# Kernel tuning notes

Hardware: AMD Instinct MI355X
Metric: run time of the kernel (lower is better)

## Reference

```python
import jax, jax.numpy as jnp
import numpy as np

EMB = 512
HEAD = 8
HEAD_DIM = EMB // HEAD


def setup_inputs() -> dict:
    key = jax.random.key(0)
    ks = jax.random.split(key, 12)
    B, S = 2, 4096
    scale = 1.0 / np.sqrt(EMB)
    inp = {
        "q": jax.random.normal(ks[0], (B, S, EMB), dtype=jnp.float32),
        "kv": jax.random.normal(ks[1], (B, S, EMB), dtype=jnp.float32),
        "Wq": jax.random.normal(ks[2], (EMB, EMB), dtype=jnp.float32) * scale,
        "bq": jax.random.normal(ks[3], (EMB,), dtype=jnp.float32) * 0.01,
        "Wk": jax.random.normal(ks[4], (EMB, EMB), dtype=jnp.float32) * scale,
        "bk": jax.random.normal(ks[5], (EMB,), dtype=jnp.float32) * 0.01,
        "Wv": jax.random.normal(ks[6], (EMB, EMB), dtype=jnp.float32) * scale,
        "bv": jax.random.normal(ks[7], (EMB,), dtype=jnp.float32) * 0.01,
        "Wo": jax.random.normal(ks[8], (EMB, EMB), dtype=jnp.float32) * scale,
        "bo": jax.random.normal(ks[9], (EMB,), dtype=jnp.float32) * 0.01,
    }
    return inp


def reference(q, kv, Wq, bq, Wk, bk, Wv, bv, Wo, bo):
    B, N, _ = q.shape
    M = kv.shape[1]
    # Linear projections (torch Linear: x @ W^T + b)
    qh = (q @ Wq.T + bq).reshape(B, N, HEAD, HEAD_DIM).transpose(0, 2, 1, 3)  # [B,H,N,d]
    kh = (kv @ Wk.T + bk).reshape(B, M, HEAD, HEAD_DIM).transpose(0, 2, 1, 3)  # [B,H,M,d]
    vh = (kv @ Wv.T + bv).reshape(B, M, HEAD, HEAD_DIM).transpose(0, 2, 1, 3)  # [B,H,M,d]
    attn = jnp.einsum("bhnd,bhmd->bhnm", qh, kh) / jnp.sqrt(jnp.float32(HEAD_DIM))
    attn = jax.nn.softmax(attn, axis=-1)
    out = jnp.einsum("bhnm,bhmd->bhnd", attn, vh)  # [B,H,N,d]
    out = out.transpose(0, 2, 1, 3).reshape(B, N, EMB)
    out = out @ Wo.T + bo
    return out
```

## Files before the change

kernel.cpp:

```cpp
#include <hip/hip_runtime.h>
#include <stdint.h>

typedef unsigned short u16;
typedef __attribute__((ext_vector_type(8))) short short8;
typedef __attribute__((ext_vector_type(4))) float f32x4;
typedef __attribute__((ext_vector_type(16))) float f32x16;

typedef __attribute__((address_space(1))) void as1_void;
typedef __attribute__((address_space(3))) void as3_void;

__device__ inline u16 f2bf(float x) {
  uint32_t u = __float_as_uint(x);
  return (u16)((u + 0x7fffu + ((u >> 16) & 1u)) >> 16);
}

__device__ inline void gload16(const void* g, void* l) {
  __builtin_amdgcn_global_load_lds((as1_void*)g, (as3_void*)l, 16, 0, 0);
}

__device__ inline uint32_t cvtpk(float lo, float hi) {
  uint32_t d;
  asm("v_cvt_pk_bf16_f32 %0, %1, %2" : "=v"(d) : "v"(lo), "v"(hi));
  return d;
}

__device__ inline void plswap(uint32_t& a, uint32_t& b) {
  asm("v_permlane32_swap_b32 %0, %1" : "+v"(a), "+v"(b));
}

__device__ inline float fexp2(float x) {
  float r;
  asm("v_exp_f32 %0, %1" : "=v"(r) : "v"(x));
  return r;
}

__global__ __launch_bounds__(256) void cvt_all(const float* __restrict__ q,
                                               const float* __restrict__ kv,
                                               const float* __restrict__ Wq,
                                               const float* __restrict__ Wk,
                                               const float* __restrict__ Wv,
                                               const float* __restrict__ Wo,
                                               u16* __restrict__ qb,
                                               u16* __restrict__ kvb,
                                               u16* __restrict__ wall) {
  const int bx = blockIdx.x;
  const float* in;
  u16* out;
  int i;
  if (bx < 4096) {
    in = q; out = qb; i = bx * 256 + threadIdx.x;
  } else if (bx < 8192) {
    in = kv; out = kvb; i = (bx - 4096) * 256 + threadIdx.x;
  } else {
    int widx = (bx - 8192) >> 8;
    in = (widx == 0) ? Wq : (widx == 1) ? Wk : (widx == 2) ? Wv : Wo;
    out = wall + (size_t)widx * 262144;
    i = ((bx - 8192) & 255) * 256 + threadIdx.x;
  }
  float4 v = ((const float4*)in)[i];
  ushort4 o;
  o.x = f2bf(v.x); o.y = f2bf(v.y); o.z = f2bf(v.z); o.w = f2bf(v.w);
  ((ushort4*)out)[i] = o;
}

__global__ __launch_bounds__(256) void gemm_qkv(const u16* __restrict__ qb,
                                                const u16* __restrict__ kvb,
                                                const u16* __restrict__ wq,
                                                const u16* __restrict__ wk,
                                                const u16* __restrict__ wv,
                                                const float* __restrict__ bq,
                                                const float* __restrict__ bk,
                                                const float* __restrict__ bv,
                                                u16* __restrict__ Qh,
                                                u16* __restrict__ Kh,
                                                u16* __restrict__ Vt, float qscale) {
  __shared__ u16 Al[128 * 32];
  __shared__ u16 Wl[128 * 32];
  const int z = blockIdx.z;
  const u16* A = (z == 0) ? qb : kvb;
  const u16* W = (z == 0) ? wq : (z == 1) ? wk : wv;
  const float* bias = (z == 0) ? bq : (z == 1) ? bk : bv;
  const float prescale = (z == 0) ? qscale : 1.0f;
  u16* Cout = (z == 0) ? Qh : (z == 1) ? Kh : Vt;

  const int tid = threadIdx.x;
  const int lane = tid & 63;
  const int wv_ = tid >> 6;
  const int c = lane & 15;
  const int g = lane >> 4;
  const int wr = wv_ >> 1, wc = wv_ & 1;
  const int m0 = blockIdx.x * 128;
  const int n0 = blockIdx.y * 128;

  f32x4 acc[4][4];
#pragma unroll
  for (int i = 0; i < 4; i++)
#pragma unroll
    for (int j = 0; j < 4; j++) acc[i][j] = (f32x4){0.f, 0.f, 0.f, 0.f};

  for (int kk = 0; kk < 512; kk += 32) {
    __syncthreads();
    {
      int t0 = tid;
      int r0 = t0 >> 2, c0 = t0 & 3;
      gload16(A + (size_t)(m0 + r0) * 512 + kk + c0 * 8, (char*)Al + (size_t)(wv_ * 64) * 16);
      gload16(W + (size_t)(n0 + r0) * 512 + kk + c0 * 8, (char*)Wl + (size_t)(wv_ * 64) * 16);
      int t1 = 256 + tid;
      int r1 = t1 >> 2, c1 = t1 & 3;
      gload16(A + (size_t)(m0 + r1) * 512 + kk + c1 * 8, (char*)Al + (size_t)(256 + wv_ * 64) * 16);
      gload16(W + (size_t)(n0 + r1) * 512 + kk + c1 * 8, (char*)Wl + (size_t)(256 + wv_ * 64) * 16);
    }
    __syncthreads();

    short8 af[4], wf[4];
#pragma unroll
    for (int ai = 0; ai < 4; ai++)
      af[ai] = *(const short8*)&Al[(wr * 64 + ai * 16 + c) * 32 + g * 8];
#pragma unroll
    for (int bj = 0; bj < 4; bj++)
      wf[bj] = *(const short8*)&Wl[(wc * 64 + bj * 16 + c) * 32 + g * 8];
#pragma unroll
    for (int ai = 0; ai < 4; ai++)
#pragma unroll
      for (int bj = 0; bj < 4; bj++)
        acc[ai][bj] = __builtin_amdgcn_mfma_f32_16x16x32_bf16(af[ai], wf[bj], acc[ai][bj], 0, 0, 0);
  }

#pragma unroll
  for (int ai = 0; ai < 4; ai++)
#pragma unroll
    for (int bj = 0; bj < 4; bj++)
#pragma unroll
      for (int r = 0; r < 4; r++) {
        int m = m0 + wr * 64 + ai * 16 + g * 4 + r;
        int n = n0 + wc * 64 + bj * 16 + c;
        float v = (acc[ai][bj][r] + bias[n]) * prescale;
        int b = m >> 12, s = m & 4095;
        int h = n >> 6, d = n & 63;
        size_t idx;
        if (z < 2)
          idx = ((size_t)(b * 8 + h) * 4096 + s) * 64 + d;
        else
          idx = ((size_t)(b * 8 + h) * 64 + d) * 4096 + s;
        Cout[idx] = f2bf(v);
      }
}

__global__ __launch_bounds__(256) void gemm_out(const u16* __restrict__ A,
                                                const u16* __restrict__ W,
                                                const float* __restrict__ bias,
                                                float* __restrict__ Cout) {
  __shared__ u16 Al[128 * 32];
  __shared__ u16 Wl[128 * 32];
  const int tid = threadIdx.x;
  const int lane = tid & 63;
  const int wv_ = tid >> 6;
  const int c = lane & 15;
  const int g = lane >> 4;
  const int wr = wv_ >> 1, wc = wv_ & 1;
  const int m0 = blockIdx.x * 128;
  const int n0 = blockIdx.y * 128;

  f32x4 acc[4][4];
#pragma unroll
  for (int i = 0; i < 4; i++)
#pragma unroll
    for (int j = 0; j < 4; j++) acc[i][j] = (f32x4){0.f, 0.f, 0.f, 0.f};

  for (int kk = 0; kk < 512; kk += 32) {
    __syncthreads();
    {
      int t0 = tid;
      int r0 = t0 >> 2, c0 = t0 & 3;
      gload16(A + (size_t)(m0 + r0) * 512 + kk + c0 * 8, (char*)Al + (size_t)(wv_ * 64) * 16);
      gload16(W + (size_t)(n0 + r0) * 512 + kk + c0 * 8, (char*)Wl + (size_t)(wv_ * 64) * 16);
      int t1 = 256 + tid;
      int r1 = t1 >> 2, c1 = t1 & 3;
      gload16(A + (size_t)(m0 + r1) * 512 + kk + c1 * 8, (char*)Al + (size_t)(256 + wv_ * 64) * 16);
      gload16(W + (size_t)(n0 + r1) * 512 + kk + c1 * 8, (char*)Wl + (size_t)(256 + wv_ * 64) * 16);
    }
    __syncthreads();

    short8 af[4], wf[4];
#pragma unroll
    for (int ai = 0; ai < 4; ai++)
      af[ai] = *(const short8*)&Al[(wr * 64 + ai * 16 + c) * 32 + g * 8];
#pragma unroll
    for (int bj = 0; bj < 4; bj++)
      wf[bj] = *(const short8*)&Wl[(wc * 64 + bj * 16 + c) * 32 + g * 8];
#pragma unroll
    for (int ai = 0; ai < 4; ai++)
#pragma unroll
      for (int bj = 0; bj < 4; bj++)
        acc[ai][bj] = __builtin_amdgcn_mfma_f32_16x16x32_bf16(af[ai], wf[bj], acc[ai][bj], 0, 0, 0);
  }

#pragma unroll
  for (int ai = 0; ai < 4; ai++)
#pragma unroll
    for (int bj = 0; bj < 4; bj++)
#pragma unroll
      for (int r = 0; r < 4; r++) {
        int m = m0 + wr * 64 + ai * 16 + g * 4 + r;
        int n = n0 + wc * 64 + bj * 16 + c;
        Cout[(size_t)m * 512 + n] = acc[ai][bj][r] + bias[n];
      }
}

__global__ __launch_bounds__(256) void attn_split(const u16* __restrict__ Qh,
                                                  const u16* __restrict__ Kh,
                                                  const u16* __restrict__ Vt,
                                                  float* __restrict__ Op,
                                                  float* __restrict__ Ml) {
  __shared__ __align__(16) char smem[32768];
  const int tid = threadIdx.x;
  const int lane = tid & 63;
  const int w = tid >> 6;
  const int c5 = lane & 31;
  const int h = lane >> 5;
  const int bid = (blockIdx.x & 7) * 128 + (blockIdx.x >> 3);
  const int half = bid & 1;
  const int qt = (bid >> 1) & 31;
  const int bh = bid >> 6;
  const int q0 = qt * 128 + w * 32;
  const u16* Qb = Qh + (size_t)bh * 262144;
  const u16* Kb = Kh + (size_t)bh * 262144 + (size_t)half * 2048 * 64;
  const u16* Vb = Vt + (size_t)bh * 262144 + half * 2048;

  short8 qf[4];
#pragma unroll
  for (int kd = 0; kd < 4; kd++)
    qf[kd] = *(const short8*)(Qb + (size_t)(q0 + c5) * 64 + kd * 16 + h * 8);

  f32x16 accO[2];
#pragma unroll
  for (int i = 0; i < 16; i++) { accO[0][i] = 0.f; accO[1][i] = 0.f; }
  float l_r = 0.f;

  const int r = tid >> 4, p = tid & 15;
  const int x = p ^ r;
  const int gb = x >> 3, ge = x & 7;
  const u16* srcKA = Kb + (size_t)(r + 32 * gb) * 64 + ge * 8;
  const u16* srcKB = Kb + (size_t)(16 + r + 32 * gb) * 64 + ge * 8;
  const u16* srcVA = Vb + (size_t)(r + 32 * gb) * 4096 + ge * 8;
  const u16* srcVB = Vb + (size_t)(16 + r + 32 * gb) * 4096 + ge * 8;

#define ATTN_STAGE(BUF, T)                                \
  {                                                       \
    char* b_ = (char*)smem + (BUF)*16384 + w * 1024;      \
    gload16(srcKA + (size_t)(T)*4096, b_);                \
    gload16(srcKB + (size_t)(T)*4096, b_ + 4096);         \
    gload16(srcVA + (T)*64, b_ + 8192);                   \
    gload16(srcVB + (T)*64, b_ + 12288);                  \
  }

  ATTN_STAGE(0, 0)
  __syncthreads();
  const int swz = c5 & 15;
  const int rowb = c5 * 128;

  short8 pa_prev[4];
  short8 vf_prev[8];

  for (int t = 0; t < 32; ++t) {
    const int cur = t & 1;
    if (t < 31) ATTN_STAGE(cur ^ 1, t + 1)

    const u16* Kl = (const u16*)(smem + cur * 16384);
    const u16* Vl = Kl + 4096;

    f32x16 s0, s1;
#pragma unroll
    for (int i = 0; i < 16; i++) { s0[i] = 0.f; s1[i] = 0.f; }
    __builtin_amdgcn_s_setprio(1);
#pragma unroll
    for (int kd = 0; kd < 4; kd++) {
      short8 kf0 = *(const short8*)&Kl[rowb + ((((kd << 1) + h) ^ swz) << 3)];
      short8 kf1 = *(const short8*)&Kl[rowb + (((8 + (kd << 1) + h) ^ swz) << 3)];
      s0 = __builtin_amdgcn_mfma_f32_32x32x16_bf16(kf0, qf[kd], s0, 0, 0, 0);
      s1 = __builtin_amdgcn_mfma_f32_32x32x16_bf16(kf1, qf[kd], s1, 0, 0, 0);
    }
    if (t > 0) {
#pragma unroll
      for (int km = 0; km < 4; km++) {
        accO[0] = __builtin_amdgcn_mfma_f32_32x32x16_bf16(vf_prev[2 * km], pa_prev[km], accO[0], 0, 0, 0);
        accO[1] = __builtin_amdgcn_mfma_f32_32x32x16_bf16(vf_prev[2 * km + 1], pa_prev[km], accO[1], 0, 0, 0);
      }
    }
    __builtin_amdgcn_s_setprio(0);
    __builtin_amdgcn_sched_barrier(0);

#pragma unroll
    for (int i = 0; i < 16; i++) { s0[i] = fexp2(s0[i]); s1[i] = fexp2(s1[i]); }

    float tsum0 = ((s0[0] + s1[0]) + (s0[4] + s1[4])) + ((s0[8] + s1[8]) + (s0[12] + s1[12]));
    float tsum1 = ((s0[1] + s1[1]) + (s0[5] + s1[5])) + ((s0[9] + s1[9]) + (s0[13] + s1[13]));
    float tsum2 = ((s0[2] + s1[2]) + (s0[6] + s1[6])) + ((s0[10] + s1[10]) + (s0[14] + s1[14]));
    float tsum3 = ((s0[3] + s1[3]) + (s0[7] + s1[7])) + ((s0[11] + s1[11]) + (s0[15] + s1[15]));
    float rsq = (tsum0 + tsum1) + (tsum2 + tsum3);
    l_r += rsq + __shfl_xor(rsq, 32);

    uint32_t pk0[4][2], pk1[4][2];
#pragma unroll
    for (int u = 0; u < 4; u++) {
      pk0[u][0] = cvtpk(s0[4 * u], s0[4 * u + 1]);
      pk0[u][1] = cvtpk(s0[4 * u + 2], s0[4 * u + 3]);
      pk1[u][0] = cvtpk(s1[4 * u], s1[4 * u + 1]);
      pk1[u][1] = cvtpk(s1[4 * u + 2], s1[4 * u + 3]);
    }
#pragma unroll
    for (int km = 0; km < 2; km++) {
      const int uA = (km & 1) * 2, uB = uA + 1;
      uint32_t a0 = pk0[uA][0], b0 = pk0[uB][0]; plswap(a0, b0);
      uint32_t a1 = pk0[uA][1], b1 = pk0[uB][1]; plswap(a1, b1);
      union { uint32_t u[4]; short8 s; } uu;
      uu.u[0] = a0; uu.u[1] = a1; uu.u[2] = b0; uu.u[3] = b1;
      pa_prev[km] = uu.s;
    }
#pragma unroll
    for (int km = 2; km < 4; km++) {
      const int uA = (km & 1) * 2, uB = uA + 1;
      uint32_t a0 = pk1[uA][0], b0 = pk1[uB][0]; plswap(a0, b0);
      uint32_t a1 = pk1[uA][1], b1 = pk1[uB][1]; plswap(a1, b1);
      union { uint32_t u[4]; short8 s; } uu;
      uu.u[0] = a0; uu.u[1] = a1; uu.u[2] = b0; uu.u[3] = b1;
      pa_prev[km] = uu.s;
    }

#pragma unroll
    for (int km = 0; km < 4; km++) {
      vf_prev[2 * km]     = *(const short8*)&Vl[rowb + ((((km << 1) + h) ^ swz) << 3)];
      vf_prev[2 * km + 1] = *(const short8*)&Vl[rowb + (((8 + (km << 1) + h) ^ swz) << 3)];
    }

    __syncthreads();
  }

#pragma unroll
  for (int km = 0; km < 4; km++) {
    accO[0] = __builtin_amdgcn_mfma_f32_32x32x16_bf16(vf_prev[2 * km], pa_prev[km], accO[0], 0, 0, 0);
    accO[1] = __builtin_amdgcn_mfma_f32_32x32x16_bf16(vf_prev[2 * km + 1], pa_prev[km], accO[1], 0, 0, 0);
  }

  const size_t pbase = (size_t)(half * 16 + bh) * 4096 + q0 + c5;
  float* Opw = Op + pbase * 64;
#pragma unroll
  for (int db = 0; db < 2; db++)
#pragma unroll
    for (int rr = 0; rr < 16; rr++) {
      int d = db * 32 + 4 * h + (rr & 3) + 8 * (rr >> 2);
      Opw[d] = accO[db][rr];
    }
  if (h == 0) { Ml[pbase * 2] = 0.f; Ml[pbase * 2 + 1] = l_r; }
}

__global__ __launch_bounds__(256) void attn_combine(const float* __restrict__ Op,
                                                    const float* __restrict__ Ml,
                                                    u16* __restrict__ aO) {
  int tg = blockIdx.x * 256 + threadIdx.x;
  int bhq = tg >> 3, seg = tg & 7;
  const float* p0 = Op + (size_t)bhq * 64 + seg * 8;
  const float* p1 = p0 + 4194304;
  float m0 = Ml[bhq * 2], l0 = Ml[bhq * 2 + 1];
  float m1 = Ml[131072 + bhq * 2], l1 = Ml[131072 + bhq * 2 + 1];
  float ms = fmaxf(m0, m1);
  float a0 = fexp2(m0 - ms), a1 = fexp2(m1 - ms);
  float inv = 1.f / (l0 * a0 + l1 * a1);
  float4 x0 = ((const float4*)p0)[0], x1 = ((const float4*)p0)[1];
  float4 y0 = ((const float4*)p1)[0], y1 = ((const float4*)p1)[1];
  ushort4 o0, o1;
  o0.x = f2bf((x0.x * a0 + y0.x * a1) * inv);
  o0.y = f2bf((x0.y * a0 + y0.y * a1) * inv);
  o0.z = f2bf((x0.z * a0 + y0.z * a1) * inv);
  o0.w = f2bf((x0.w * a0 + y0.w * a1) * inv);
  o1.x = f2bf((x1.x * a0 + y1.x * a1) * inv);
  o1.y = f2bf((x1.y * a0 + y1.y * a1) * inv);
  o1.z = f2bf((x1.z * a0 + y1.z * a1) * inv);
  o1.w = f2bf((x1.w * a0 + y1.w * a1) * inv);
  int bh = bhq >> 12, q = bhq & 4095;
  int b = bh >> 3, hh = bh & 7;
  u16* dst = aO + ((size_t)(b * 4096 + q)) * 512 + hh * 64 + seg * 8;
  ((ushort4*)dst)[0] = o0;
  ((ushort4*)dst)[1] = o1;
}

extern "C" void kernel_launch(void* const* d_in, const int* in_sizes, int n_in,
                              void* d_out, int out_size, void* d_ws, size_t ws_size,
                              hipStream_t stream) {
  const float* q  = (const float*)d_in[0];
  const float* kv = (const float*)d_in[1];
  const float* Wq = (const float*)d_in[2];
  const float* bq = (const float*)d_in[3];
  const float* Wk = (const float*)d_in[4];
  const float* bk = (const float*)d_in[5];
  const float* Wv = (const float*)d_in[6];
  const float* bv = (const float*)d_in[7];
  const float* Wo = (const float*)d_in[8];
  const float* bo = (const float*)d_in[9];

  const size_t MB = 1u << 20;
  char* ws = (char*)d_ws;
  u16* qb  = (u16*)(ws + 0 * MB);
  u16* kvb = (u16*)(ws + 8 * MB);
  u16* wqb = (u16*)(ws + 16 * MB);
  u16* wkb = (u16*)(ws + 16 * MB + 524288);
  u16* wvb = (u16*)(ws + 17 * MB);
  u16* wob = (u16*)(ws + 17 * MB + 524288);
  u16* Qh  = (u16*)(ws + 18 * MB);
  u16* Kh  = (u16*)(ws + 26 * MB);
  u16* Vt  = (u16*)(ws + 34 * MB);
  u16* aO  = (u16*)(ws + 42 * MB);
  float* Op = (float*)(ws + 50 * MB);
  float* Ml = (float*)(ws + 84 * MB);

  cvt_all<<<dim3(9216), dim3(256), 0, stream>>>(q, kv, Wq, Wk, Wv, Wo, qb, kvb, wqb);

  const float qscale = 0.125f * 1.44269504088896340736f;
  gemm_qkv<<<dim3(64, 4, 3), dim3(256), 0, stream>>>(qb, kvb, wqb, wkb, wvb,
                                                     bq, bk, bv, Qh, Kh, Vt, qscale);

  attn_split<<<dim3(1024), dim3(256), 0, stream>>>(Qh, Kh, Vt, Op, Ml);
  attn_combine<<<dim3(2048), dim3(256), 0, stream>>>(Op, Ml, aO);

  gemm_out<<<dim3(64, 4), dim3(256), 0, stream>>>(aO, wob, bo, (float*)d_out);
}
```

Measured before the change: 142.6 us.

## Double-buffer GEMM K loop with swizzled LDS and smaller M tiles

Both projection GEMMs now prefetch the next 64-wide K slice into a second LDS buffer while computing on the current one, so each iteration needs one barrier instead of two. The shared tiles use an XOR swizzle to avoid LDS bank conflicts. The M tile shrinks from 128 to 64, doubling the grid to fill more CUs. This uses 48KB LDS per block, which may lower occupancy, and smaller tiles reduce reuse of the weight tile.

```diff
diff --git a/kernel.cpp b/kernel.cpp
--- a/kernel.cpp
+++ b/kernel.cpp
@@ -74,8 +74,7 @@
                                                 u16* __restrict__ Qh,
                                                 u16* __restrict__ Kh,
                                                 u16* __restrict__ Vt, float qscale) {
-  __shared__ u16 Al[128 * 32];
-  __shared__ u16 Wl[128 * 32];
+  __shared__ __align__(16) char smem[49152];
   const int z = blockIdx.z;
   const u16* A = (z == 0) ? qb : kvb;
   const u16* W = (z == 0) ? wq : (z == 1) ? wk : wv;
@@ -89,50 +88,65 @@
   const int c = lane & 15;
   const int g = lane >> 4;
   const int wr = wv_ >> 1, wc = wv_ & 1;
-  const int m0 = blockIdx.x * 128;
+  const int m0 = blockIdx.x * 64;
   const int n0 = blockIdx.y * 128;
 
-  f32x4 acc[4][4];
-#pragma unroll
-  for (int i = 0; i < 4; i++)
+  const int r0 = tid >> 3, cc = tid & 7;
+  const int u0 = cc ^ (r0 & 7);
+  const u16* srcA0 = A + (size_t)(m0 + r0) * 512 + u0 * 8;
+  const u16* srcW0 = W + (size_t)(n0 + r0) * 512 + u0 * 8;
+
+#define GEMM_STAGE(BUF, KK)                              \
+  {                                                      \
+    char* ab_ = (char*)smem + (BUF)*24576 + wv_ * 1024;  \
+    gload16(srcA0 + (KK), ab_);                          \
+    gload16(srcA0 + (KK) + 16384, ab_ + 4096);           \
+    gload16(srcW0 + (KK), ab_ + 8192);                   \
+    gload16(srcW0 + (KK) + 16384, ab_ + 12288);          \
+    gload16(srcW0 + (KK) + 32768, ab_ + 16384);          \
+    gload16(srcW0 + (KK) + 49152, ab_ + 20480);          \
+  }
+
+  f32x4 acc[2][4];
+#pragma unroll
+  for (int i = 0; i < 2; i++)
 #pragma unroll
     for (int j = 0; j < 4; j++) acc[i][j] = (f32x4){0.f, 0.f, 0.f, 0.f};
 
-  for (int kk = 0; kk < 512; kk += 32) {
+  GEMM_STAGE(0, 0)
+  __syncthreads();
+  int cur = 0;
+  const int swa = c & 7;
+  for (int it = 0; it < 8; ++it) {
+    if (it < 7) GEMM_STAGE(cur ^ 1, (it + 1) * 64)
+    const u16* Ab = (const u16*)((char*)smem + cur * 24576);
+    const u16* Wb = Ab + 4096;
+#pragma unroll
+    for (int kd = 0; kd < 2; kd++) {
+      short8 af[2], wf[4];
+#pragma unroll
+      for (int ai = 0; ai < 2; ai++)
+        af[ai] = *(const short8*)&Ab[(wr * 32 + ai * 16 + c) * 64 + (((kd * 4 + g) ^ swa) << 3)];
+#pragma unroll
+      for (int bj = 0; bj < 4; bj++)
+        wf[bj] = *(const short8*)&Wb[(wc * 64 + bj * 16 + c) * 64 + (((kd * 4 + g) ^ swa) << 3)];
+#pragma unroll
+      for (int ai = 0; ai < 2; ai++)
+#pragma unroll
+        for (int bj = 0; bj < 4; bj++)
+          acc[ai][bj] = __builtin_amdgcn_mfma_f32_16x16x32_bf16(af[ai], wf[bj], acc[ai][bj], 0, 0, 0);
+    }
     __syncthreads();
-    {
-      int t0 = tid;
-      int r0 = t0 >> 2, c0 = t0 & 3;
-      gload16(A + (size_t)(m0 + r0) * 512 + kk + c0 * 8, (char*)Al + (size_t)(wv_ * 64) * 16);
-      gload16(W + (size_t)(n0 + r0) * 512 + kk + c0 * 8, (char*)Wl + (size_t)(wv_ * 64) * 16);
-      int t1 = 256 + tid;
-      int r1 = t1 >> 2, c1 = t1 & 3;
-      gload16(A + (size_t)(m0 + r1) * 512 + kk + c1 * 8, (char*)Al + (size_t)(256 + wv_ * 64) * 16);
-      gload16(W + (size_t)(n0 + r1) * 512 + kk + c1 * 8, (char*)Wl + (size_t)(256 + wv_ * 64) * 16);
-    }
-    __syncthreads();
-
-    short8 af[4], wf[4];
-#pragma unroll
-    for (int ai = 0; ai < 4; ai++)
-      af[ai] = *(const short8*)&Al[(wr * 64 + ai * 16 + c) * 32 + g * 8];
+    cur ^= 1;
+  }
+
+#pragma unroll
+  for (int ai = 0; ai < 2; ai++)
 #pragma unroll
     for (int bj = 0; bj < 4; bj++)
-      wf[bj] = *(const short8*)&Wl[(wc * 64 + bj * 16 + c) * 32 + g * 8];
-#pragma unroll
-    for (int ai = 0; ai < 4; ai++)
-#pragma unroll
-      for (int bj = 0; bj < 4; bj++)
-        acc[ai][bj] = __builtin_amdgcn_mfma_f32_16x16x32_bf16(af[ai], wf[bj], acc[ai][bj], 0, 0, 0);
-  }
-
-#pragma unroll
-  for (int ai = 0; ai < 4; ai++)
-#pragma unroll
-    for (int bj = 0; bj < 4; bj++)
 #pragma unroll
       for (int r = 0; r < 4; r++) {
-        int m = m0 + wr * 64 + ai * 16 + g * 4 + r;
+        int m = m0 + wr * 32 + ai * 16 + g * 4 + r;
         int n = n0 + wc * 64 + bj * 16 + c;
         float v = (acc[ai][bj][r] + bias[n]) * prescale;
         int b = m >> 12, s = m & 4095;
@@ -150,58 +164,61 @@
                                                 const u16* __restrict__ W,
                                                 const float* __restrict__ bias,
                                                 float* __restrict__ Cout) {
-  __shared__ u16 Al[128 * 32];
-  __shared__ u16 Wl[128 * 32];
+  __shared__ __align__(16) char smem[49152];
   const int tid = threadIdx.x;
   const int lane = tid & 63;
   const int wv_ = tid >> 6;
   const int c = lane & 15;
   const int g = lane >> 4;
   const int wr = wv_ >> 1, wc = wv_ & 1;
-  const int m0 = blockIdx.x * 128;
+  const int m0 = blockIdx.x * 64;
   const int n0 = blockIdx.y * 128;
 
-  f32x4 acc[4][4];
-#pragma unroll
-  for (int i = 0; i < 4; i++)
+  const int r0 = tid >> 3, cc = tid & 7;
+  const int u0 = cc ^ (r0 & 7);
+  const u16* srcA0 = A + (size_t)(m0 + r0) * 512 + u0 * 8;
+  const u16* srcW0 = W + (size_t)(n0 + r0) * 512 + u0 * 8;
+
+  f32x4 acc[2][4];
+#pragma unroll
+  for (int i = 0; i < 2; i++)
 #pragma unroll
     for (int j = 0; j < 4; j++) acc[i][j] = (f32x4){0.f, 0.f, 0.f, 0.f};
 
-  for (int kk = 0; kk < 512; kk += 32) {
+  GEMM_STAGE(0, 0)
+  __syncthreads();
+  int cur = 0;
+  const int swa = c & 7;
+  for (int it = 0; it < 8; ++it) {
+    if (it < 7) GEMM_STAGE(cur ^ 1, (it + 1) * 64)
+    const u16* Ab = (const u16*)((char*)smem + cur * 24576);
+    const u16* Wb = Ab + 4096;
+#pragma unroll
+    for (int kd = 0; kd < 2; kd++) {
+      short8 af[2], wf[4];
+#pragma unroll
+      for (int ai = 0; ai < 2; ai++)
+        af[ai] = *(const short8*)&Ab[(wr * 32 + ai * 16 + c) * 64 + (((kd * 4 + g) ^ swa) << 3)];
+#pragma unroll
+      for (int bj = 0; bj < 4; bj++)
+        wf[bj] = *(const short8*)&Wb[(wc * 64 + bj * 16 + c) * 64 + (((kd * 4 + g) ^ swa) << 3)];
+#pragma unroll
+      for (int ai = 0; ai < 2; ai++)
+#pragma unroll
+        for (int bj = 0; bj < 4; bj++)
+          acc[ai][bj] = __builtin_amdgcn_mfma_f32_16x16x32_bf16(af[ai], wf[bj], acc[ai][bj], 0, 0, 0);
+    }
     __syncthreads();
-    {
-      int t0 = tid;
-      int r0 = t0 >> 2, c0 = t0 & 3;
-      gload16(A + (size_t)(m0 + r0) * 512 + kk + c0 * 8, (char*)Al + (size_t)(wv_ * 64) * 16);
-      gload16(W + (size_t)(n0 + r0) * 512 + kk + c0 * 8, (char*)Wl + (size_t)(wv_ * 64) * 16);
-      int t1 = 256 + tid;
-      int r1 = t1 >> 2, c1 = t1 & 3;
-      gload16(A + (size_t)(m0 + r1) * 512 + kk + c1 * 8, (char*)Al + (size_t)(256 + wv_ * 64) * 16);
-      gload16(W + (size_t)(n0 + r1) * 512 + kk + c1 * 8, (char*)Wl + (size_t)(256 + wv_ * 64) * 16);
-    }
-    __syncthreads();
-
-    short8 af[4], wf[4];
-#pragma unroll
-    for (int ai = 0; ai < 4; ai++)
-      af[ai] = *(const short8*)&Al[(wr * 64 + ai * 16 + c) * 32 + g * 8];
+    cur ^= 1;
+  }
+
+#pragma unroll
+  for (int ai = 0; ai < 2; ai++)
 #pragma unroll
     for (int bj = 0; bj < 4; bj++)
-      wf[bj] = *(const short8*)&Wl[(wc * 64 + bj * 16 + c) * 32 + g * 8];
-#pragma unroll
-    for (int ai = 0; ai < 4; ai++)
-#pragma unroll
-      for (int bj = 0; bj < 4; bj++)
-        acc[ai][bj] = __builtin_amdgcn_mfma_f32_16x16x32_bf16(af[ai], wf[bj], acc[ai][bj], 0, 0, 0);
-  }
-
-#pragma unroll
-  for (int ai = 0; ai < 4; ai++)
-#pragma unroll
-    for (int bj = 0; bj < 4; bj++)
 #pragma unroll
       for (int r = 0; r < 4; r++) {
-        int m = m0 + wr * 64 + ai * 16 + g * 4 + r;
+        int m = m0 + wr * 32 + ai * 16 + g * 4 + r;
         int n = n0 + wc * 64 + bj * 16 + c;
         Cout[(size_t)m * 512 + n] = acc[ai][bj][r] + bias[n];
       }
@@ -416,11 +433,11 @@
   cvt_all<<<dim3(9216), dim3(256), 0, stream>>>(q, kv, Wq, Wk, Wv, Wo, qb, kvb, wqb);
 
   const float qscale = 0.125f * 1.44269504088896340736f;
-  gemm_qkv<<<dim3(64, 4, 3), dim3(256), 0, stream>>>(qb, kvb, wqb, wkb, wvb,
-                                                     bq, bk, bv, Qh, Kh, Vt, qscale);
+  gemm_qkv<<<dim3(128, 4, 3), dim3(256), 0, stream>>>(qb, kvb, wqb, wkb, wvb,
+                                                      bq, bk, bv, Qh, Kh, Vt, qscale);
 
   attn_split<<<dim3(1024), dim3(256), 0, stream>>>(Qh, Kh, Vt, Op, Ml);
   attn_combine<<<dim3(2048), dim3(256), 0, stream>>>(Op, Ml, aO);
 
-  gemm_out<<<dim3(64, 4), dim3(256), 0, stream>>>(aO, wob, bo, (float*)d_out);
-}
+  gemm_out<<<dim3(128, 4), dim3(256), 0, stream>>>(aO, wob, bo, (float*)d_out);
+}
```

Measured after the change: 140.0 us. No clear change (-1.9%).
